# Kernel tuning notes

Measured on AMD Instinct MI355X. Metric: run time of the kernel, lower is better.

## Reference

```python
import jax, jax.numpy as jnp
import numpy as np

C = 640      # in_channels == out_channels (required by source: same generator applied to both)
K = 3        # kernel_size
R = int(C * 0.2)  # reduction hidden = 128
H = 10
W = 10
BS = 25      # support: 5-way 5-shot
BQ = 75      # query: 5-way 15-query


def setup_inputs() -> dict:
    key = jax.random.key(0)
    ks = jax.random.split(key, 16)
    s = 0.02  # weight scale to keep the 4-deep linear chain numerically tame
    rn = lambda k, shape: jax.random.normal(k, shape, jnp.float32) * s
    return {
        "support_set": jax.random.normal(ks[0], (BS, C, H, W), jnp.float32),
        "query_set": jax.random.normal(ks[1], (BQ, C, H, W), jnp.float32),
        # ContextLearningModule: four 1x1 convs (no nonlinearity in source)
        "Wc1": rn(ks[2], (C, C)), "bc1": jnp.zeros((C,), jnp.float32),
        "Wc2": rn(ks[3], (C, C)), "bc2": jnp.zeros((C,), jnp.float32),
        "Wc3": rn(ks[4], (C, C)), "bc3": jnp.zeros((C,), jnp.float32),
        "Wc4": rn(ks[5], (C, C)), "bc4": jnp.zeros((C,), jnp.float32),
        # DynamicKernelGenerator channel branch: Linear(C,R) -> ReLU -> Linear(R, C*K*K)
        "W1": rn(ks[6], (C, R)), "b1": jnp.zeros((R,), jnp.float32),
        "W2": rn(ks[7], (R, C * K * K)), "b2": jnp.zeros((C * K * K,), jnp.float32),
        # DynamicKernelGenerator spatial branch: Conv2d(C, K*K, 1)
        "Ws": rn(ks[8], (K * K, C)), "bs": jnp.zeros((K * K,), jnp.float32),
    }


def _conv1x1(x, Wt, b):
    # x: [b, c, h, w], Wt: [o, c]
    return jnp.einsum('bchw,oc->bohw', x, Wt) + b[None, :, None, None]


def _dyn_kernel(x, W1, b1, W2, b2, Ws, bs):
    # x: [b, C, h, w] -> per-pixel dynamic kernel [b, C, h, w, K, K]
    b, c, h, w = x.shape
    pooled = x.mean(axis=(2, 3))  # adaptive_avg_pool2d(...,1)
    ck = jax.nn.relu(pooled @ W1 + b1) @ W2 + b2          # [b, C*K*K]
    ck = ck.reshape(b, c, K, K)                            # channel kernel
    sk = jnp.einsum('bchw,kc->bkhw', x, Ws) + bs[None, :, None, None]
    sk = sk.reshape(b, h, w, K, K)                         # raw view, as in source
    return ck[:, :, None, None, :, :] * sk[:, None, :, :, :, :]


def _involution(x, kernel):
    # x: [b, C, h, w]; kernel: [b or 1, C, h, w, K, K]
    # out[b,c,i,j] = sum_{u,v} kernel[b,c,i,j,u,v] * x[b,c,i+u-p, j+v-p]
    h, w = x.shape[-2:]
    p = K // 2
    xp = jnp.pad(x, ((0, 0), (0, 0), (p, p), (p, p)))
    return sum(kernel[..., u, v] * xp[:, :, u:u + h, v:v + w]
               for u in range(K) for v in range(K))


def reference(support_set, query_set, Wc1, bc1, Wc2, bc2, Wc3, bc3, Wc4, bc4,
              W1, b1, W2, b2, Ws, bs):
    sf, qf = support_set, query_set  # identity backbone
    # context learning module
    tsr = _conv1x1(_conv1x1(_conv1x1(_conv1x1(sf, Wc1, bc1), Wc2, bc2), Wc3, bc3), Wc4, bc4)
    # task-specific kernel, averaged over the support batch -> [1, C, H, W, K, K]
    task_kernel = _dyn_kernel(tsr, W1, b1, W2, b2, Ws, bs).mean(axis=0, keepdims=True)
    # per-instance kernels (batched; identical math to the per-sample loop)
    inst_kernels = _dyn_kernel(sf, W1, b1, W2, b2, Ws, bs)  # [BS, C, H, W, K, K]
    fused = inst_kernels * task_kernel
    adapted_support = _involution(sf, fused)        # [BS, C, H, W]
    adapted_query = _involution(qf, task_kernel)    # [BQ, C, H, W] (kernel broadcast)
    return (adapted_support, adapted_query)
```

## Files before the change

kernel.cpp:

```cpp
#include <hip/hip_runtime.h>

#define CCH   640
#define RDIM  128
#define HWPIX 100
#define NBS   25
#define NBQ   75
#define CKK   5760
#define SF_B  64000

#define OFF_PG0  0
#define OFF_PGA  16000
#define OFF_PGB  32000
#define OFF_ATA  48000
#define OFF_ATB  53760
#define OFF_BA   59520
#define OFF_BB   59536
#define OFF_HP   59552
#define OFF_SKT  85152
#define OFF_SKS  130152
#define OFF_SKSC 175152
#define OFF_CKT  197652
#define OFF_CKS  341652
#define OFF_TASK 485652

__global__ void pool_kernel(const float* __restrict__ sf, float* __restrict__ Pg0) {
    int idx = blockIdx.x * 64 + threadIdx.x;
    if (idx >= NBS * CCH) return;
    int b = idx / CCH, c = idx % CCH;
    const float4* s4 = (const float4*)(sf + b * SF_B + c * HWPIX);
    float acc = 0.f;
#pragma unroll
    for (int q = 0; q < 25; ++q) {
        float4 v = s4[q];
        acc += (v.x + v.y) + (v.z + v.w);
    }
    Pg0[idx] = acc * 0.01f;
}

__global__ void chain_step(const float* __restrict__ Pin, const float* __restrict__ Wp,
                           const float* __restrict__ bp, float* __restrict__ Pout,
                           const float* __restrict__ Ain, const float* __restrict__ Wa,
                           const float* __restrict__ ba, const float* __restrict__ Bin,
                           float* __restrict__ Aout, float* __restrict__ Bout,
                           int first, const float* __restrict__ Ws, const float* __restrict__ bs) {
    __shared__ float red[256];
    int blk = blockIdx.x, t = threadIdx.x;
    int lane = t & 63;
    if (blk < 4000) {
        int W = blk * 4 + (t >> 6);
        int o = W / NBS, b = W % NBS;
        const float2* w2 = (const float2*)(Wp + o * CCH);
        const float2* p2 = (const float2*)(Pin + b * CCH);
        float acc = 0.f;
#pragma unroll
        for (int s = 0; s < 5; ++s) {
            float2 wv = w2[s * 64 + lane];
            float2 pv = p2[s * 64 + lane];
            acc += wv.x * pv.x + wv.y * pv.y;
        }
#pragma unroll
        for (int m = 32; m >= 1; m >>= 1) acc += __shfl_xor(acc, m);
        if (lane == 0) Pout[b * CCH + o] = acc + bp[o];
    } else if (blk < 4090) {
        int w = blk - 4000;
        int k = w / 10, ctile = w % 10;
        int og = t >> 6, cl = lane;
        int c = ctile * 64 + cl;
        int o0 = og * 160;
        float acc = 0.f;
        if (first) {
            const float* ar = Ws + k * CCH;
#pragma unroll 8
            for (int o = o0; o < o0 + 160; ++o)
                acc += ar[o] * Wa[o * CCH + c];
        } else {
#pragma unroll 8
            for (int o = o0; o < o0 + 160; ++o)
                acc += Ain[o * 9 + k] * Wa[o * CCH + c];
        }
        red[t] = acc;
        __syncthreads();
        if (t < 64) {
            float s = red[t] + red[64 + t] + red[128 + t] + red[192 + t];
            Aout[(ctile * 64 + t) * 9 + k] = s;
        }
    } else {
        int WB = (blk - 4090) * 4 + (t >> 6);
        if (WB >= 9) return;
        int k = WB;
        float acc = 0.f;
        if (first) {
            const float* ar = Ws + k * CCH;
#pragma unroll
            for (int s = 0; s < 10; ++s) acc += ar[s * 64 + lane] * ba[s * 64 + lane];
        } else {
#pragma unroll
            for (int s = 0; s < 10; ++s) acc += Ain[(s * 64 + lane) * 9 + k] * ba[s * 64 + lane];
        }
#pragma unroll
        for (int m = 32; m >= 1; m >>= 1) acc += __shfl_xor(acc, m);
        if (lane == 0) Bout[k] = acc + (first ? bs[k] : Bin[k]);
    }
}

__global__ void postchain(const float* __restrict__ sf, const float* __restrict__ Pg0,
                          const float* __restrict__ Pgf, const float* __restrict__ W1,
                          float* __restrict__ Hp, const float* __restrict__ A4T,
                          const float* __restrict__ betaF, const float* __restrict__ Ws,
                          const float* __restrict__ bs, float* __restrict__ SKT,
                          float* __restrict__ SKS) {
    int blk = blockIdx.x, t = threadIdx.x;
    if (blk < 100) {
        int pair = blk / 2;
        int s = (blk % 2) * 2 + (t >> 7);
        int r = t & 127;
        int branch = pair / NBS, b = pair % NBS;
        const float* prow = (branch ? Pg0 : Pgf) + b * CCH;
        int c0 = s * 160;
        float acc = 0.f;
#pragma unroll 8
        for (int c = 0; c < 160; ++c)
            acc += prow[c0 + c] * W1[(c0 + c) * RDIM + r];
        Hp[(pair * 4 + s) * RDIM + r] = acc;
    } else {
        int sidx = (blk - 100) * 256 + t;
        if (sidx >= 45000) return;
        int s = sidx / 22500;
        int rem = sidx % 22500;
        int b = rem / 900;
        int r2 = rem % 900;
        int k = r2 / HWPIX, q = r2 % HWPIX;
        const float* x = sf + b * SF_B + q;
        const float* wsr = Ws + k * CCH;
        int c0 = s * 320;
        float acc0 = 0.f, acc1 = 0.f;
#pragma unroll 8
        for (int c = 0; c < 320; ++c) {
            float xc = x[(c0 + c) * HWPIX];
            acc0 += A4T[(c0 + c) * 9 + k] * xc;
            acc1 += wsr[c0 + c] * xc;
        }
        if (s == 0) { acc0 += betaF[k]; acc1 += bs[k]; }
        SKT[sidx] = acc0;
        SKS[sidx] = acc1;
    }
}

__global__ void mlp_phase2(const float* __restrict__ Hp, const float* __restrict__ b1,
                           const float* __restrict__ W2, const float* __restrict__ b2,
                           float* __restrict__ ckt, float* __restrict__ cks) {
    __shared__ float hs[RDIM];
    int pair = blockIdx.x / 9, chunk = blockIdx.x % 9;
    int t = threadIdx.x;
    int branch = pair / NBS, b = pair % NBS;
    if (t < RDIM) {
        const float* hp = Hp + pair * 4 * RDIM;
        hs[t] = fmaxf(b1[t] + hp[t] + hp[RDIM + t] + hp[2 * RDIM + t] + hp[3 * RDIM + t], 0.f);
    }
    __syncthreads();
    int jbase = chunk * 640;
    float acc0 = b2[jbase + t], acc1 = b2[jbase + t + 320];
#pragma unroll 4
    for (int r = 0; r < RDIM; ++r) {
        const float* wrow = W2 + r * CKK + jbase;
        float h = hs[r];
        acc0 += h * wrow[t];
        acc1 += h * wrow[t + 320];
    }
    float* ck = (branch ? cks : ckt) + b * CKK + jbase;
    ck[t] = acc0;
    ck[t + 320] = acc1;
}

__global__ void task_assemble(const float* __restrict__ ckt, const float* __restrict__ SKT,
                              const float* __restrict__ SKS, float* __restrict__ task,
                              float* __restrict__ SKSc) {
    int blk = blockIdx.x, t = threadIdx.x;
    if (blk < 2250) {
        int idx = blk * 256 + t;
        if (idx >= CCH * 900) return;
        int c = idx / 900;
        int r = idx % 900;
        int uv = idx % 9;
        float acc = 0.f;
#pragma unroll
        for (int b = 0; b < NBS; ++b)
            acc += ckt[b * CKK + c * 9 + uv] * (SKT[b * 900 + r] + SKT[22500 + b * 900 + r]);
        task[idx] = acc * 0.04f;
    } else {
        int cidx = (blk - 2250) * 256 + t;
        if (cidx >= 22500) return;
        SKSc[cidx] = SKS[cidx] + SKS[22500 + cidx];
    }
}

__global__ __launch_bounds__(256, 4) void involutions(
        const float* __restrict__ sf, const float* __restrict__ qf,
        const float* __restrict__ task, const float* __restrict__ cks,
        const float* __restrict__ sksc, float* __restrict__ out) {
    __shared__ float lds[8 * 900 + 900 + 72];
    float* tk_l = lds;
    float* sv_l = lds + 7200;
    float* cv_l = lds + 8100;
    int blk = blockIdx.x, t = threadIdx.x;
    if (blk < 2000) {
        int b = blk / 80, cg = blk % 80;
        int c0 = cg * 8;
        for (int r = t; r < 7200; r += 256) tk_l[r] = task[c0 * 900 + r];
        for (int r = t; r < 900; r += 256) sv_l[r] = sksc[b * 900 + r];
        if (t < 72) cv_l[t] = cks[b * CKK + c0 * 9 + t];
        __syncthreads();
        const float* xb = sf + b * SF_B;
        float* ob = out + b * SF_B;
#pragma unroll
        for (int it = 0; it < 4; ++it) {
            int item = it * 256 + t;
            if (item >= 800) break;
            int cl = item / 100, p = item % 100;
            int i = p / 10, j = p % 10;
            const float* x = xb + (c0 + cl) * HWPIX;
            const float* tkp = tk_l + cl * 900 + p * 9;
            const float* svp = sv_l + p * 9;
            const float* cvp = cv_l + cl * 9;
            float acc = 0.f;
#pragma unroll
            for (int u = 0; u < 3; ++u) {
                int ii = i + u - 1;
                bool rowok = (ii >= 0) && (ii <= 9);
#pragma unroll
                for (int v = 0; v < 3; ++v) {
                    int jj = j + v - 1;
                    bool ok = rowok && (jj >= 0) && (jj <= 9);
                    float xv = ok ? x[ii * 10 + jj] : 0.f;
                    int uv = u * 3 + v;
                    acc += cvp[uv] * svp[uv] * tkp[uv] * xv;
                }
            }
            ob[(c0 + cl) * HWPIX + p] = acc;
        }
    } else {
        int qb = blk - 2000;
        int c = qb / 3, bg = qb % 3;
        for (int r = t; r < 900; r += 256) tk_l[r] = task[c * 900 + r];
        __syncthreads();
#pragma unroll
        for (int it = 0; it < 10; ++it) {
            int item = it * 256 + t;
            if (item >= 2500) break;
            int bl = item / 100, p = item % 100;
            int b = bg * 25 + bl;
            int i = p / 10, j = p % 10;
            const float* x = qf + b * SF_B + c * HWPIX;
            const float* tkp = tk_l + p * 9;
            float acc = 0.f;
#pragma unroll
            for (int u = 0; u < 3; ++u) {
                int ii = i + u - 1;
                bool rowok = (ii >= 0) && (ii <= 9);
#pragma unroll
                for (int v = 0; v < 3; ++v) {
                    int jj = j + v - 1;
                    bool ok = rowok && (jj >= 0) && (jj <= 9);
                    float xv = ok ? x[ii * 10 + jj] : 0.f;
                    acc += tkp[u * 3 + v] * xv;
                }
            }
            out[NBS * SF_B + b * SF_B + c * HWPIX + p] = acc;
        }
    }
}

extern "C" void kernel_launch(void* const* d_in, const int* in_sizes, int n_in,
                              void* d_out, int out_size, void* d_ws, size_t ws_size,
                              hipStream_t stream) {
    const float* sf  = (const float*)d_in[0];
    const float* qf  = (const float*)d_in[1];
    const float* Wc[4] = {(const float*)d_in[2], (const float*)d_in[4],
                          (const float*)d_in[6], (const float*)d_in[8]};
    const float* bc[4] = {(const float*)d_in[3], (const float*)d_in[5],
                          (const float*)d_in[7], (const float*)d_in[9]};
    const float* W1 = (const float*)d_in[10];
    const float* b1 = (const float*)d_in[11];
    const float* W2 = (const float*)d_in[12];
    const float* b2 = (const float*)d_in[13];
    const float* Ws = (const float*)d_in[14];
    const float* bs = (const float*)d_in[15];
    float* out = (float*)d_out;
    float* ws = (float*)d_ws;

    float* Pg0 = ws + OFF_PG0;
    float* Pga = ws + OFF_PGA;
    float* Pgb = ws + OFF_PGB;
    float* ATa = ws + OFF_ATA;
    float* ATb = ws + OFF_ATB;
    float* Ba  = ws + OFF_BA;
    float* Bb  = ws + OFF_BB;
    float* Hp  = ws + OFF_HP;
    float* SKT = ws + OFF_SKT;
    float* SKS = ws + OFF_SKS;
    float* SKSc= ws + OFF_SKSC;
    float* CKT = ws + OFF_CKT;
    float* CKS = ws + OFF_CKS;
    float* TSK = ws + OFF_TASK;

    pool_kernel<<<250, 64, 0, stream>>>(sf, Pg0);

    chain_step<<<4093, 256, 0, stream>>>(Pg0, Wc[0], bc[0], Pga, nullptr, Wc[3], bc[3], nullptr,
                                         ATa, Ba, 1, Ws, bs);
    chain_step<<<4093, 256, 0, stream>>>(Pga, Wc[1], bc[1], Pgb, ATa, Wc[2], bc[2], Ba,
                                         ATb, Bb, 0, Ws, bs);
    chain_step<<<4093, 256, 0, stream>>>(Pgb, Wc[2], bc[2], Pga, ATb, Wc[1], bc[1], Bb,
                                         ATa, Ba, 0, Ws, bs);
    chain_step<<<4093, 256, 0, stream>>>(Pga, Wc[3], bc[3], Pgb, ATa, Wc[0], bc[0], Ba,
                                         ATb, Bb, 0, Ws, bs);

    postchain<<<276, 256, 0, stream>>>(sf, Pg0, Pgb, W1, Hp, ATb, Bb, Ws, bs, SKT, SKS);
    mlp_phase2<<<450, 320, 0, stream>>>(Hp, b1, W2, b2, CKT, CKS);
    task_assemble<<<2338, 256, 0, stream>>>(CKT, SKT, SKS, TSK, SKSc);
    involutions<<<3920, 256, 0, stream>>>(sf, qf, TSK, CKS, SKSc, out);
}
```

Baseline: 241.6 us.

## Transpose kernel buffers to uv-major layout and flatten involution to one thread per output

Stores spatial kernels, the task kernel and the summed support spatial kernel in uv-major, pixel-contiguous layouts, so that reads in the involution are coalesced across pixels. The involution kernel drops the LDS staging and per-block channel grouping and uses one thread per output element with clamped, masked neighbour loads. The MLP phase-2 kernel computes both branches per block, so each W2 row is read once for both. This trades LDS reuse of the task kernel for coalesced global and cache reads, and launches many more small blocks.

```diff
diff --git a/kernel.cpp b/kernel.cpp
--- a/kernel.cpp
+++ b/kernel.cpp
@@ -8,20 +8,20 @@
 #define CKK   5760
 #define SF_B  64000
 
-#define OFF_PG0  0
-#define OFF_PGA  16000
-#define OFF_PGB  32000
-#define OFF_ATA  48000
-#define OFF_ATB  53760
-#define OFF_BA   59520
-#define OFF_BB   59536
-#define OFF_HP   59552
-#define OFF_SKT  85152
-#define OFF_SKS  130152
-#define OFF_SKSC 175152
-#define OFF_CKT  197652
-#define OFF_CKS  341652
-#define OFF_TASK 485652
+#define OFF_PG0   0
+#define OFF_PGA   16000
+#define OFF_PGB   32000
+#define OFF_ATA   48000
+#define OFF_ATB   53760
+#define OFF_BA    59520
+#define OFF_BB    59536
+#define OFF_HP    59552
+#define OFF_SKT   85152
+#define OFF_SKS   130152
+#define OFF_SKSCT 175152
+#define OFF_CKT   197652
+#define OFF_CKS   341652
+#define OFF_TASKT 485652
 
 __global__ void pool_kernel(const float* __restrict__ sf, float* __restrict__ Pg0) {
     int idx = blockIdx.x * 64 + threadIdx.x;
@@ -141,133 +141,107 @@
             acc1 += wsr[c0 + c] * xc;
         }
         if (s == 0) { acc0 += betaF[k]; acc1 += bs[k]; }
-        SKT[sidx] = acc0;
-        SKS[sidx] = acc1;
+        int p = r2 / 9, uv = r2 % 9;
+        int dst = s * 22500 + b * 900 + uv * 100 + p;
+        SKT[dst] = acc0;
+        SKS[dst] = acc1;
     }
 }
 
 __global__ void mlp_phase2(const float* __restrict__ Hp, const float* __restrict__ b1,
                            const float* __restrict__ W2, const float* __restrict__ b2,
                            float* __restrict__ ckt, float* __restrict__ cks) {
-    __shared__ float hs[RDIM];
-    int pair = blockIdx.x / 9, chunk = blockIdx.x % 9;
+    __shared__ float hs0[RDIM], hs1[RDIM];
+    int b = blockIdx.x / 9, chunk = blockIdx.x % 9;
     int t = threadIdx.x;
-    int branch = pair / NBS, b = pair % NBS;
     if (t < RDIM) {
-        const float* hp = Hp + pair * 4 * RDIM;
-        hs[t] = fmaxf(b1[t] + hp[t] + hp[RDIM + t] + hp[2 * RDIM + t] + hp[3 * RDIM + t], 0.f);
+        const float* hp = Hp + b * 4 * RDIM;
+        hs0[t] = fmaxf(b1[t] + hp[t] + hp[RDIM + t] + hp[2 * RDIM + t] + hp[3 * RDIM + t], 0.f);
+    } else if (t < 2 * RDIM) {
+        int r = t - RDIM;
+        const float* hp = Hp + (NBS + b) * 4 * RDIM;
+        hs1[r] = fmaxf(b1[r] + hp[r] + hp[RDIM + r] + hp[2 * RDIM + r] + hp[3 * RDIM + r], 0.f);
     }
     __syncthreads();
     int jbase = chunk * 640;
-    float acc0 = b2[jbase + t], acc1 = b2[jbase + t + 320];
+    float a00 = b2[jbase + t], a01 = b2[jbase + t + 320];
+    float a10 = a00, a11 = a01;
 #pragma unroll 4
     for (int r = 0; r < RDIM; ++r) {
         const float* wrow = W2 + r * CKK + jbase;
-        float h = hs[r];
-        acc0 += h * wrow[t];
-        acc1 += h * wrow[t + 320];
-    }
-    float* ck = (branch ? cks : ckt) + b * CKK + jbase;
-    ck[t] = acc0;
-    ck[t + 320] = acc1;
+        float w0 = wrow[t], w1 = wrow[t + 320];
+        float h0 = hs0[r], h1 = hs1[r];
+        a00 += h0 * w0; a01 += h0 * w1;
+        a10 += h1 * w0; a11 += h1 * w1;
+    }
+    float* c0 = ckt + b * CKK + jbase;
+    float* c1 = cks + b * CKK + jbase;
+    c0[t] = a00; c0[t + 320] = a01;
+    c1[t] = a10; c1[t + 320] = a11;
 }
 
 __global__ void task_assemble(const float* __restrict__ ckt, const float* __restrict__ SKT,
-                              const float* __restrict__ SKS, float* __restrict__ task,
-                              float* __restrict__ SKSc) {
+                              const float* __restrict__ SKS, float* __restrict__ taskT,
+                              float* __restrict__ sksT) {
     int blk = blockIdx.x, t = threadIdx.x;
     if (blk < 2250) {
         int idx = blk * 256 + t;
-        if (idx >= CCH * 900) return;
-        int c = idx / 900;
-        int r = idx % 900;
-        int uv = idx % 9;
+        int uv = idx / 64000;
+        int rem = idx % 64000;
+        int c = rem / 100, p = rem % 100;
         float acc = 0.f;
 #pragma unroll
         for (int b = 0; b < NBS; ++b)
-            acc += ckt[b * CKK + c * 9 + uv] * (SKT[b * 900 + r] + SKT[22500 + b * 900 + r]);
-        task[idx] = acc * 0.04f;
+            acc += ckt[b * CKK + c * 9 + uv] *
+                   (SKT[b * 900 + uv * 100 + p] + SKT[22500 + b * 900 + uv * 100 + p]);
+        taskT[idx] = acc * 0.04f;
     } else {
         int cidx = (blk - 2250) * 256 + t;
         if (cidx >= 22500) return;
-        SKSc[cidx] = SKS[cidx] + SKS[22500 + cidx];
-    }
-}
-
-__global__ __launch_bounds__(256, 4) void involutions(
+        int uv = cidx / 2500;
+        int r = cidx % 2500;
+        int src = (r / 100) * 900 + uv * 100 + (r % 100);
+        sksT[cidx] = SKS[src] + SKS[22500 + src];
+    }
+}
+
+__global__ __launch_bounds__(256) void involutions(
         const float* __restrict__ sf, const float* __restrict__ qf,
-        const float* __restrict__ task, const float* __restrict__ cks,
-        const float* __restrict__ sksc, float* __restrict__ out) {
-    __shared__ float lds[8 * 900 + 900 + 72];
-    float* tk_l = lds;
-    float* sv_l = lds + 7200;
-    float* cv_l = lds + 8100;
-    int blk = blockIdx.x, t = threadIdx.x;
-    if (blk < 2000) {
-        int b = blk / 80, cg = blk % 80;
-        int c0 = cg * 8;
-        for (int r = t; r < 7200; r += 256) tk_l[r] = task[c0 * 900 + r];
-        for (int r = t; r < 900; r += 256) sv_l[r] = sksc[b * 900 + r];
-        if (t < 72) cv_l[t] = cks[b * CKK + c0 * 9 + t];
-        __syncthreads();
-        const float* xb = sf + b * SF_B;
-        float* ob = out + b * SF_B;
-#pragma unroll
-        for (int it = 0; it < 4; ++it) {
-            int item = it * 256 + t;
-            if (item >= 800) break;
-            int cl = item / 100, p = item % 100;
-            int i = p / 10, j = p % 10;
-            const float* x = xb + (c0 + cl) * HWPIX;
-            const float* tkp = tk_l + cl * 900 + p * 9;
-            const float* svp = sv_l + p * 9;
-            const float* cvp = cv_l + cl * 9;
-            float acc = 0.f;
-#pragma unroll
-            for (int u = 0; u < 3; ++u) {
-                int ii = i + u - 1;
-                bool rowok = (ii >= 0) && (ii <= 9);
-#pragma unroll
-                for (int v = 0; v < 3; ++v) {
-                    int jj = j + v - 1;
-                    bool ok = rowok && (jj >= 0) && (jj <= 9);
-                    float xv = ok ? x[ii * 10 + jj] : 0.f;
-                    int uv = u * 3 + v;
-                    acc += cvp[uv] * svp[uv] * tkp[uv] * xv;
-                }
-            }
-            ob[(c0 + cl) * HWPIX + p] = acc;
-        }
-    } else {
-        int qb = blk - 2000;
-        int c = qb / 3, bg = qb % 3;
-        for (int r = t; r < 900; r += 256) tk_l[r] = task[c * 900 + r];
-        __syncthreads();
-#pragma unroll
-        for (int it = 0; it < 10; ++it) {
-            int item = it * 256 + t;
-            if (item >= 2500) break;
-            int bl = item / 100, p = item % 100;
-            int b = bg * 25 + bl;
-            int i = p / 10, j = p % 10;
-            const float* x = qf + b * SF_B + c * HWPIX;
-            const float* tkp = tk_l + p * 9;
-            float acc = 0.f;
-#pragma unroll
-            for (int u = 0; u < 3; ++u) {
-                int ii = i + u - 1;
-                bool rowok = (ii >= 0) && (ii <= 9);
-#pragma unroll
-                for (int v = 0; v < 3; ++v) {
-                    int jj = j + v - 1;
-                    bool ok = rowok && (jj >= 0) && (jj <= 9);
-                    float xv = ok ? x[ii * 10 + jj] : 0.f;
-                    acc += tkp[u * 3 + v] * xv;
-                }
-            }
-            out[NBS * SF_B + b * SF_B + c * HWPIX + p] = acc;
-        }
-    }
+        const float* __restrict__ taskT, const float* __restrict__ cks,
+        const float* __restrict__ sksT, float* __restrict__ out) {
+    int idx = blockIdx.x * 256 + threadIdx.x;
+    bool support = idx < NBS * SF_B;
+    int b, c, p;
+    const float* x;
+    if (support) {
+        b = idx / SF_B; int rem = idx % SF_B; c = rem / 100; p = rem % 100;
+        x = sf + b * SF_B + c * 100;
+    } else {
+        int qidx = idx - NBS * SF_B;
+        b = qidx / SF_B; int rem = qidx % SF_B; c = rem / 100; p = rem % 100;
+        x = qf + b * SF_B + c * 100;
+    }
+    int i = p / 10, j = p % 10;
+    float acc = 0.f;
+#pragma unroll
+    for (int u = 0; u < 3; ++u) {
+        int ii = i + u - 1;
+        float mrow = ((unsigned)ii < 10u) ? 1.f : 0.f;
+        int ci = min(max(ii, 0), 9);
+#pragma unroll
+        for (int v = 0; v < 3; ++v) {
+            int jj = j + v - 1;
+            float m = ((unsigned)jj < 10u) ? mrow : 0.f;
+            int cj = min(max(jj, 0), 9);
+            float xv = x[ci * 10 + cj] * m;
+            int uv = u * 3 + v;
+            float w = taskT[uv * 64000 + c * 100 + p];
+            if (support)
+                w *= cks[b * CKK + c * 9 + uv] * sksT[uv * 2500 + b * 100 + p];
+            acc += w * xv;
+        }
+    }
+    out[idx] = acc;
 }
 
 extern "C" void kernel_launch(void* const* d_in, const int* in_sizes, int n_in,
@@ -298,10 +272,10 @@
     float* Hp  = ws + OFF_HP;
     float* SKT = ws + OFF_SKT;
     float* SKS = ws + OFF_SKS;
-    float* SKSc= ws + OFF_SKSC;
+    float* SKsT= ws + OFF_SKSCT;
     float* CKT = ws + OFF_CKT;
     float* CKS = ws + OFF_CKS;
-    float* TSK = ws + OFF_TASK;
+    float* TKT = ws + OFF_TASKT;
 
     pool_kernel<<<250, 64, 0, stream>>>(sf, Pg0);
 
@@ -315,7 +289,7 @@
                                          ATb, Bb, 0, Ws, bs);
 
     postchain<<<276, 256, 0, stream>>>(sf, Pg0, Pgb, W1, Hp, ATb, Bb, Ws, bs, SKT, SKS);
-    mlp_phase2<<<450, 320, 0, stream>>>(Hp, b1, W2, b2, CKT, CKS);
-    task_assemble<<<2338, 256, 0, stream>>>(CKT, SKT, SKS, TSK, SKSc);
-    involutions<<<3920, 256, 0, stream>>>(sf, qf, TSK, CKS, SKSc, out);
-}
+    mlp_phase2<<<225, 320, 0, stream>>>(Hp, b1, W2, b2, CKT, CKS);
+    task_assemble<<<2338, 256, 0, stream>>>(CKT, SKT, SKS, TKT, SKsT);
+    involutions<<<25000, 256, 0, stream>>>(sf, qf, TKT, CKS, SKsT, out);
+}
```

New measurement: 231.3 us. 1.04x faster.
